# Kernel optimization log

Hardware: AMD Instinct MI355X
Metric: run time of the kernel (lower is better)

## Reference

```python
import jax, jax.numpy as jnp
import numpy as np

D = 1024        # embed_size
F = 4096        # ffn_dim
E = 8           # n_experts
K = 2           # top_k_experts
NS = 1          # n_shared
T = 8192        # tokens


def setup_inputs() -> dict:
    key = jax.random.key(0)
    ks = jax.random.split(key, 12)
    s = lambda *sh: 1.0 / np.sqrt(sh[-2] if len(sh) > 1 else sh[-1])
    inp = {
        "x": jax.random.normal(ks[0], (T, D), jnp.float32),
        "gate_w": jax.random.normal(ks[1], (D, E), jnp.float32) * (1.0 / np.sqrt(D)),
        "gate_b": jnp.zeros((E,), jnp.float32),
        "shared_w1": jax.random.normal(ks[2], (NS, D, 2 * F), jnp.float32) * (1.0 / np.sqrt(D)),
        "shared_b1": jnp.zeros((NS, 2 * F), jnp.float32),
        "shared_w2": jax.random.normal(ks[3], (NS, F, D), jnp.float32) * (1.0 / np.sqrt(F)),
        "shared_b2": jnp.zeros((NS, D), jnp.float32),
        "routed_w1": jax.random.normal(ks[4], (E, D, 2 * F), jnp.float32) * (1.0 / np.sqrt(D)),
        "routed_b1": jnp.zeros((E, 2 * F), jnp.float32),
        "routed_w2": jax.random.normal(ks[5], (E, F, D), jnp.float32) * (1.0 / np.sqrt(F)),
        "routed_b2": jnp.zeros((E, D), jnp.float32),
    }
    return inp


def _expert(x, w1, b1, w2, b2):
    # SwiGLU FFN: w2( silu(a) * b ) where [a, b] = chunk(x @ w1 + b1)
    h = x @ w1 + b1                      # [T, 2F]
    a, b = jnp.split(h, 2, axis=-1)      # [T, F] each
    return (jax.nn.silu(a) * b) @ w2 + b2  # [T, D]


def reference(x, gate_w, gate_b, shared_w1, shared_b1, shared_w2, shared_b2,
              routed_w1, routed_b1, routed_w2, routed_b2):
    # shared experts (always active)
    shared_out = jnp.zeros_like(x)
    for i in range(NS):
        shared_out = shared_out + _expert(x, shared_w1[i], shared_b1[i], shared_w2[i], shared_b2[i])

    # softmax gating + top-k selection
    logits = x @ gate_w + gate_b                      # [T, E]
    probs = jax.nn.softmax(logits, axis=-1)
    topk_probs, topk_idx = jax.lax.top_k(probs, K)    # [T, K]

    # per-token combine weight for each expert: sum_k p_k * 1[idx_k == e]
    one_hot = jax.nn.one_hot(topk_idx, E, dtype=x.dtype)        # [T, K, E]
    combine = jnp.einsum("tk,tke->te", topk_probs, one_hot)     # [T, E]

    # dispatch/combine: dense per-expert FFN, weighted by combine (zero off-route)
    routed_out = jnp.zeros_like(x)
    for e in range(E):
        y = _expert(x, routed_w1[e], routed_b1[e], routed_w2[e], routed_b2[e])
        routed_out = routed_out + y * combine[:, e:e + 1]

    return shared_out + routed_out
```

## Files before the change

kernel.cpp:

```cpp
#include <hip/hip_runtime.h>

#define TOK   8192
#define DD    1024
#define FF    4096
#define EE    8
#define TWOF  8192
#define NSLOT 16384
#define PADT  17408

typedef unsigned short u16;
typedef float  f32x16 __attribute__((ext_vector_type(16)));
typedef __bf16 bf16x8 __attribute__((ext_vector_type(8)));

__device__ __forceinline__ u16 f2b(float f) {
  unsigned u = __builtin_bit_cast(unsigned, f);
  u += 0x7fffu + ((u >> 16) & 1u);
  return (u16)(u >> 16);
}

__device__ __forceinline__ float b2f(u16 b) {
  return __builtin_bit_cast(float, (unsigned)b << 16);
}

__device__ __forceinline__ void ldslds16(const void* g, void* l) {
  __builtin_amdgcn_global_load_lds((const __attribute__((address_space(1))) void*)g,
                                   (__attribute__((address_space(3))) void*)l, 16, 0, 0);
}

__global__ void gate_kernel(const float* __restrict__ x, const float* __restrict__ gw,
                            const float* __restrict__ gb, int* __restrict__ counts,
                            int* __restrict__ eidx, int* __restrict__ epos,
                            float* __restrict__ ew, u16* __restrict__ xb) {
  const int wave = threadIdx.x >> 6, lane = threadIdx.x & 63;
  const int t = blockIdx.x * 4 + wave;
  float acc[EE] = {0,0,0,0,0,0,0,0};
  const float* xr = x + (size_t)t * DD;
  u16* xbr = xb + (size_t)t * DD;
#pragma unroll
  for (int i = 0; i < DD / 256; ++i) {
    const int f = i * 64 + lane;
    const float4 v = ((const float4*)xr)[f];
    const int d = f * 4;
    const float* g = gw + (size_t)d * EE;
#pragma unroll
    for (int e = 0; e < EE; ++e)
      acc[e] += v.x * g[e] + v.y * g[EE + e] + v.z * g[2 * EE + e] + v.w * g[3 * EE + e];
    uint2 pk;
    pk.x = (unsigned)f2b(v.x) | ((unsigned)f2b(v.y) << 16);
    pk.y = (unsigned)f2b(v.z) | ((unsigned)f2b(v.w) << 16);
    ((uint2*)xbr)[f] = pk;
  }
#pragma unroll
  for (int e = 0; e < EE; ++e)
#pragma unroll
    for (int off = 32; off > 0; off >>= 1) acc[e] += __shfl_down(acc[e], off);
  if (lane == 0) {
    float l[EE];
#pragma unroll
    for (int e = 0; e < EE; ++e) l[e] = acc[e] + gb[e];
    int i0 = 0;
    for (int e = 1; e < EE; ++e) if (l[e] > l[i0]) i0 = e;
    int i1 = (i0 == 0) ? 1 : 0;
    for (int e = 0; e < EE; ++e) { if (e == i0) continue; if (l[e] > l[i1]) i1 = e; }
    float m = l[0];
    for (int e = 1; e < EE; ++e) m = fmaxf(m, l[e]);
    float s = 0.f, p[EE];
    for (int e = 0; e < EE; ++e) { p[e] = __expf(l[e] - m); s += p[e]; }
    float w0 = p[i0] / s, w1 = p[i1] / s;
    int p0 = atomicAdd(&counts[i0], 1);
    int p1 = atomicAdd(&counts[i1], 1);
    eidx[2*t] = i0; eidx[2*t+1] = i1;
    epos[2*t] = p0; epos[2*t+1] = p1;
    ew[2*t] = w0;  ew[2*t+1] = w1;
  }
}

__global__ void slot_kernel(const int* __restrict__ eidx, const int* __restrict__ epos,
                            const float* __restrict__ ew, const int* __restrict__ counts,
                            int* __restrict__ s2t, float* __restrict__ swt,
                            int* __restrict__ t2s) {
  int i = blockIdx.x * 256 + threadIdx.x;
  int e = eidx[i];
  int off = 0;
  for (int j = 0; j < e; ++j) off += (counts[j] + 127) & ~127;
  int slot = off + epos[i];
  s2t[slot] = i >> 1;
  swt[slot] = ew[i];
  t2s[i] = slot;
}

__global__ void wt_kernel(const float* __restrict__ srcS, const float* __restrict__ srcR,
                          u16* __restrict__ dst, int K, int N, int permute) {
  __shared__ float tile[64][65];
  const int seg = blockIdx.z;
  const float* src = (seg == 0) ? srcS : srcR + (size_t)(seg - 1) * K * N;
  const int pc0 = blockIdx.x * 64, k0 = blockIdx.y * 64;
  const int tid = threadIdx.x;
  {
    const int kk = tid >> 2;
    const float* srow = src + (size_t)(k0 + kk) * N;
#pragma unroll
    for (int c4 = 0; c4 < 4; ++c4) {
      const int j = (tid & 3) * 4 + c4 * 16;
      const int n = pc0 + j;
      const int oc = permute ? (((n >> 6) << 5) + (n & 31) + ((n & 32) ? FF : 0)) : n;
      const float4 v = *(const float4*)(srow + oc);
      tile[kk][j]     = v.x; tile[kk][j + 1] = v.y;
      tile[kk][j + 2] = v.z; tile[kk][j + 3] = v.w;
    }
  }
  __syncthreads();
  {
    const int c = tid & 7;
#pragma unroll
    for (int p = 0; p < 2; ++p) {
      const int pp = p * 32 + (tid >> 3);
      u16* drow = dst + (size_t)seg * N * K + (size_t)(pc0 + pp) * K + k0;
      uint4 v; unsigned* pv = (unsigned*)&v;
#pragma unroll
      for (int q = 0; q < 4; ++q)
        pv[q] = (unsigned)f2b(tile[c * 8 + 2 * q][pp]) |
                ((unsigned)f2b(tile[c * 8 + 2 * q + 1][pp]) << 16);
      *(uint4*)(drow + c * 8) = v;
    }
  }
}


__device__ __forceinline__ void kloop32(int niter,
    const char* a0, const char* a1, const char* a2, const char* a3,
    const char* b0, const char* b1, const char* b2, const char* b3,
    u16* As, u16* Bs, int tid, f32x16 (&acc)[2][2]) {
  const int lane = tid & 63, l31 = lane & 31, kg = (lane >> 5) * 16;
  const int wid = tid >> 6, wm = wid >> 1, wn = wid & 1;
  const int C = (l31 & 7) << 4;
  const char* rA[4]; const char* rB[4];
#pragma unroll
  for (int ks = 0; ks < 4; ++ks) {
    const int o = (ks * 32 + kg) ^ C;
    rA[ks] = (const char*)As + (wm * 64 + l31) * 128 + o;
    rB[ks] = (const char*)Bs + (wn * 64 + l31) * 128 + o;
  }
  for (int it = 0; it < niter; ++it) {
    const long long kb = (long long)it * 128;
    ldslds16(a0 + kb, As + tid * 8);
    ldslds16(a1 + kb, As + 2048 + tid * 8);
    ldslds16(a2 + kb, As + 4096 + tid * 8);
    ldslds16(a3 + kb, As + 6144 + tid * 8);
    ldslds16(b0 + kb, Bs + tid * 8);
    ldslds16(b1 + kb, Bs + 2048 + tid * 8);
    ldslds16(b2 + kb, Bs + 4096 + tid * 8);
    ldslds16(b3 + kb, Bs + 6144 + tid * 8);
    __syncthreads();
#pragma unroll
    for (int ks = 0; ks < 4; ++ks) {
      bf16x8 af0 = *(const bf16x8*)(rA[ks]);
      bf16x8 af1 = *(const bf16x8*)(rA[ks] + 4096);
      bf16x8 bq0 = *(const bf16x8*)(rB[ks]);
      bf16x8 bq1 = *(const bf16x8*)(rB[ks] + 4096);
      acc[0][0] = __builtin_amdgcn_mfma_f32_32x32x16_bf16(af0, bq0, acc[0][0], 0, 0, 0);
      acc[0][1] = __builtin_amdgcn_mfma_f32_32x32x16_bf16(af0, bq1, acc[0][1], 0, 0, 0);
      acc[1][0] = __builtin_amdgcn_mfma_f32_32x32x16_bf16(af1, bq0, acc[1][0], 0, 0, 0);
      acc[1][1] = __builtin_amdgcn_mfma_f32_32x32x16_bf16(af1, bq1, acc[1][1], 0, 0, 0);
    }
    __syncthreads();
  }
}

__device__ __forceinline__ bool seg_map(int g, const int* __restrict__ counts,
                                        int& seg, int& tm, int& rowstart, int& rows) {
  if (g < 64) { seg = 0; tm = g; rowstart = 0; rows = TOK; return true; }
  int gr = g - 64, off = 0;
  for (int e = 0; e < EE; ++e) {
    int c = counts[e];
    int nb = (c + 127) >> 7;
    if (gr < nb) { seg = e + 1; tm = gr; rowstart = off; rows = c; return true; }
    gr -= nb;
    off += (c + 127) & ~127;
  }
  return false;
}

__global__ __launch_bounds__(256, 4)
void gemm1_kernel(const u16* __restrict__ xb, const int* __restrict__ s2t,
                  const u16* __restrict__ w1t, const float* __restrict__ sb1,
                  const float* __restrict__ rb1, const int* __restrict__ counts,
                  u16* __restrict__ hs) {
  __shared__ __align__(16) u16 As[128 * 64];
  __shared__ __align__(16) u16 Bs[128 * 64];
  const int lin = blockIdx.x + 64 * blockIdx.y;
  const int tn = (lin & 7) * 8 + ((lin >> 3) & 7);
  const int g = lin >> 6;
  int seg, tm, rowstart, rows;
  if (!seg_map(g, counts, seg, tm, rowstart, rows)) return;
  const int hsbase = (seg == 0) ? 0 : TOK + rowstart;
  const int tid = threadIdx.x, lane = tid & 63, wid = tid >> 6;
  const int wm = wid >> 1, wn = wid & 1;

  const int srow = tid >> 3;
  const int scol = ((tid & 7) * 16) ^ ((srow & 7) << 4);
  const char* Ac = (const char*)xb;
  const char* Bc = (const char*)(w1t + (size_t)seg * TWOF * DD);
  const char* a[4]; const char* b[4];
#pragma unroll
  for (int r = 0; r < 4; ++r) {
    int rbase = tm * 128 + r * 32 + srow;
    int rg = (seg == 0) ? rbase : s2t[rowstart + rbase];
    a[r] = Ac + (size_t)rg * (DD * 2) + scol;
    b[r] = Bc + (size_t)(tn * 128 + r * 32 + srow) * (DD * 2) + scol;
  }

  f32x16 acc[2][2] = {};
  kloop32(DD / 64, a[0], a[1], a[2], a[3], b[0], b[1], b[2], b[3],
          As, Bs, tid, acc);

  const int l31 = lane & 31, lg = lane >> 5;
  const int rlim = rows - tm * 128;
  const float* b1 = (seg == 0) ? sb1 : rb1 + (size_t)(seg - 1) * TWOF;
  const int f = (tn * 2 + wn) * 32 + l31;
  const float ba = b1[f], bb = b1[FF + f];
  u16* hbase = hs + (size_t)(hsbase + tm * 128) * FF;
#pragma unroll
  for (int mi = 0; mi < 2; ++mi)
#pragma unroll
    for (int reg = 0; reg < 16; ++reg) {
      int lr = wm * 64 + mi * 32 + (reg & 3) + 8 * (reg >> 2) + 4 * lg;
      if (lr < rlim) {
        float av = acc[mi][0][reg] + ba;
        float bv = acc[mi][1][reg] + bb;
        float sv = av / (1.0f + __expf(-av)) * bv;
        hbase[(size_t)lr * FF + f] = f2b(sv);
      }
    }
}

__global__ __launch_bounds__(256, 4)
void gemm2_kernel(const u16* __restrict__ hs, const u16* __restrict__ w2t,
                  const float* __restrict__ sb2, const float* __restrict__ rb2,
                  const int* __restrict__ counts, u16* __restrict__ yo) {
  __shared__ __align__(16) u16 As[128 * 64];
  __shared__ __align__(16) u16 Bs[128 * 64];
  const int tn = blockIdx.x;
  const int g = blockIdx.y;
  int seg, tm, rowstart, rows;
  if (!seg_map(g, counts, seg, tm, rowstart, rows)) return;
  const int hrow0 = (seg == 0) ? 0 : TOK + rowstart;
  const int tid = threadIdx.x, lane = tid & 63, wid = tid >> 6;
  const int wm = wid >> 1, wn = wid & 1;

  const int srow = tid >> 3;
  const int scol = ((tid & 7) * 16) ^ ((srow & 7) << 4);
  const char* Ac = (const char*)hs;
  const char* Bc = (const char*)(w2t + (size_t)seg * DD * FF);
  const char* a[4]; const char* b[4];
#pragma unroll
  for (int r = 0; r < 4; ++r) {
    a[r] = Ac + (size_t)(hrow0 + tm * 128 + r * 32 + srow) * (FF * 2) + scol;
    b[r] = Bc + (size_t)(tn * 128 + r * 32 + srow) * (FF * 2) + scol;
  }

  f32x16 acc[2][2] = {};
  kloop32(FF / 64, a[0], a[1], a[2], a[3], b[0], b[1], b[2], b[3],
          As, Bs, tid, acc);

  const int l31 = lane & 31, lg = lane >> 5;
  const int rlim = rows - tm * 128;
  const float* b2 = (seg == 0) ? sb2 : rb2 + (size_t)(seg - 1) * DD;
  const int c0 = tn * 128 + wn * 64 + l31;
  const float bias0 = b2[c0], bias1 = b2[c0 + 32];
  u16* ybase = yo + (size_t)(hrow0 + tm * 128) * DD;
#pragma unroll
  for (int mi = 0; mi < 2; ++mi)
#pragma unroll
    for (int reg = 0; reg < 16; ++reg) {
      int lr = wm * 64 + mi * 32 + (reg & 3) + 8 * (reg >> 2) + 4 * lg;
      if (lr < rlim) {
        u16* orow = ybase + (size_t)lr * DD;
        orow[c0]      = f2b(acc[mi][0][reg] + bias0);
        orow[c0 + 32] = f2b(acc[mi][1][reg] + bias1);
      }
    }
}

__global__ void combine_kernel(const u16* __restrict__ yo, const int* __restrict__ t2s,
                               const float* __restrict__ ew, float* __restrict__ out) {
  const int t = blockIdx.x, d = threadIdx.x;
  const int s0 = t2s[2*t], s1 = t2s[2*t+1];
  const float w0 = ew[2*t], w1 = ew[2*t+1];
  const uint2 pa = ((const uint2*)(yo + (size_t)t * DD))[d];
  const uint2 p0 = ((const uint2*)(yo + (size_t)(TOK + s0) * DD))[d];
  const uint2 p1 = ((const uint2*)(yo + (size_t)(TOK + s1) * DD))[d];
  float4 r;
  r.x = b2f((u16)pa.x)         + w0 * b2f((u16)p0.x)         + w1 * b2f((u16)p1.x);
  r.y = b2f((u16)(pa.x >> 16)) + w0 * b2f((u16)(p0.x >> 16)) + w1 * b2f((u16)(p1.x >> 16));
  r.z = b2f((u16)pa.y)         + w0 * b2f((u16)p0.y)         + w1 * b2f((u16)p1.y);
  r.w = b2f((u16)(pa.y >> 16)) + w0 * b2f((u16)(p0.y >> 16)) + w1 * b2f((u16)(p1.y >> 16));
  ((float4*)(out + (size_t)t * DD))[d] = r;
}

extern "C" void kernel_launch(void* const* d_in, const int* in_sizes, int n_in,
                              void* d_out, int out_size, void* d_ws, size_t ws_size,
                              hipStream_t stream) {
  const float* x   = (const float*)d_in[0];
  const float* gw  = (const float*)d_in[1];
  const float* gb  = (const float*)d_in[2];
  const float* sw1 = (const float*)d_in[3];
  const float* sb1 = (const float*)d_in[4];
  const float* sw2 = (const float*)d_in[5];
  const float* sb2 = (const float*)d_in[6];
  const float* rw1 = (const float*)d_in[7];
  const float* rb1 = (const float*)d_in[8];
  const float* rw2 = (const float*)d_in[9];
  const float* rb2 = (const float*)d_in[10];
  float* out = (float*)d_out;

  char* p = (char*)d_ws;
  auto alloc = [&](size_t bytes) { char* r = p; p += (bytes + 255) & ~(size_t)255; return r; };
  int*   counts = (int*)alloc(EE * 4);
  int*   eidx   = (int*)alloc((size_t)2 * TOK * 4);
  int*   epos   = (int*)alloc((size_t)2 * TOK * 4);
  float* ew     = (float*)alloc((size_t)2 * TOK * 4);
  int*   s2t    = (int*)alloc((size_t)PADT * 4);
  float* swt    = (float*)alloc((size_t)PADT * 4);
  int*   t2s    = (int*)alloc((size_t)2 * TOK * 4);
  u16*   xb     = (u16*)alloc((size_t)TOK * DD * 2);
  u16*   w1t    = (u16*)alloc((size_t)9 * TWOF * DD * 2);
  u16*   w2t    = (u16*)alloc((size_t)9 * DD * FF * 2);
  u16*   hs     = (u16*)alloc((size_t)(TOK + PADT + 128) * FF * 2);
  u16*   yo     = (u16*)w1t;

  hipMemsetAsync(counts, 0, EE * 4, stream);
  hipMemsetAsync(s2t, 0, (size_t)PADT * 4, stream);
  gate_kernel<<<TOK / 4, 256, 0, stream>>>(x, gw, gb, counts, eidx, epos, ew, xb);
  slot_kernel<<<(2 * TOK) / 256, 256, 0, stream>>>(eidx, epos, ew, counts, s2t, swt, t2s);
  wt_kernel<<<dim3(TWOF / 64, DD / 64, 9), 256, 0, stream>>>(sw1, rw1, w1t, DD, TWOF, 1);
  wt_kernel<<<dim3(DD / 64, FF / 64, 9), 256, 0, stream>>>(sw2, rw2, w2t, FF, DD, 0);
  gemm1_kernel<<<dim3(64, 200), 256, 0, stream>>>(xb, s2t, w1t, sb1, rb1, counts, hs);
  gemm2_kernel<<<dim3(8, 200), 256, 0, stream>>>(hs, w2t, sb2, rb2, counts, yo);
  combine_kernel<<<TOK, 256, 0, stream>>>(yo, t2s, ew, out);
}
```

Measured before the change: 1.079 ms.

## Switch GEMM inner loops from 32x32x16 to 16x16x32 bf16 MFMA tiles

Replaces the 32x32x16 MFMA micro-kernel with a 4x4 grid of 16x16x32 MFMA tiles per wave. The LDS fragment addressing, the SwiGLU column permutation in the weight pre-transpose, and both GEMM epilogues change to match the new accumulator layout. Each wave now issues more fragment loads and more, smaller MFMA instructions per K step, trading instruction count and register layout against MFMA issue characteristics. The permute has to stay consistent with the epilogue pairing of a and b columns.

```diff
diff --git a/kernel.cpp b/kernel.cpp
--- a/kernel.cpp
+++ b/kernel.cpp
@@ -9,7 +9,7 @@
 #define PADT  17408
 
 typedef unsigned short u16;
-typedef float  f32x16 __attribute__((ext_vector_type(16)));
+typedef float  f32x4  __attribute__((ext_vector_type(4)));
 typedef __bf16 bf16x8 __attribute__((ext_vector_type(8)));
 
 __device__ __forceinline__ u16 f2b(float f) {
@@ -103,7 +103,7 @@
     for (int c4 = 0; c4 < 4; ++c4) {
       const int j = (tid & 3) * 4 + c4 * 16;
       const int n = pc0 + j;
-      const int oc = permute ? (((n >> 6) << 5) + (n & 31) + ((n & 32) ? FF : 0)) : n;
+      const int oc = permute ? (((n >> 5) << 4) + (n & 15) + ((n & 16) ? FF : 0)) : n;
       const float4 v = *(const float4*)(srow + oc);
       tile[kk][j]     = v.x; tile[kk][j + 1] = v.y;
       tile[kk][j + 2] = v.z; tile[kk][j + 3] = v.w;
@@ -127,41 +127,46 @@
 }
 
 
-__device__ __forceinline__ void kloop32(int niter,
+__device__ __forceinline__ void kloop16(int niter,
     const char* a0, const char* a1, const char* a2, const char* a3,
     const char* b0, const char* b1, const char* b2, const char* b3,
-    u16* As, u16* Bs, int tid, f32x16 (&acc)[2][2]) {
-  const int lane = tid & 63, l31 = lane & 31, kg = (lane >> 5) * 16;
+    u16* As, u16* Bs, int tid, f32x4 (&acc)[4][4]) {
+  const int lane = tid & 63, fr = lane & 15, kb = (lane >> 4) * 16;
   const int wid = tid >> 6, wm = wid >> 1, wn = wid & 1;
-  const int C = (l31 & 7) << 4;
-  const char* rA[4]; const char* rB[4];
-#pragma unroll
-  for (int ks = 0; ks < 4; ++ks) {
-    const int o = (ks * 32 + kg) ^ C;
-    rA[ks] = (const char*)As + (wm * 64 + l31) * 128 + o;
-    rB[ks] = (const char*)Bs + (wn * 64 + l31) * 128 + o;
+  const int swz = (fr & 7) << 4;
+  const char* rA[2][4]; const char* rB[2][4];
+#pragma unroll
+  for (int ks = 0; ks < 2; ++ks) {
+    const int o = (ks * 64 + kb) ^ swz;
+#pragma unroll
+    for (int q = 0; q < 4; ++q) {
+      rA[ks][q] = (const char*)As + (wm * 64 + q * 16 + fr) * 128 + o;
+      rB[ks][q] = (const char*)Bs + (wn * 64 + q * 16 + fr) * 128 + o;
+    }
   }
   for (int it = 0; it < niter; ++it) {
-    const long long kb = (long long)it * 128;
-    ldslds16(a0 + kb, As + tid * 8);
-    ldslds16(a1 + kb, As + 2048 + tid * 8);
-    ldslds16(a2 + kb, As + 4096 + tid * 8);
-    ldslds16(a3 + kb, As + 6144 + tid * 8);
-    ldslds16(b0 + kb, Bs + tid * 8);
-    ldslds16(b1 + kb, Bs + 2048 + tid * 8);
-    ldslds16(b2 + kb, Bs + 4096 + tid * 8);
-    ldslds16(b3 + kb, Bs + 6144 + tid * 8);
+    const long long kbb = (long long)it * 128;
+    ldslds16(a0 + kbb, As + tid * 8);
+    ldslds16(a1 + kbb, As + 2048 + tid * 8);
+    ldslds16(a2 + kbb, As + 4096 + tid * 8);
+    ldslds16(a3 + kbb, As + 6144 + tid * 8);
+    ldslds16(b0 + kbb, Bs + tid * 8);
+    ldslds16(b1 + kbb, Bs + 2048 + tid * 8);
+    ldslds16(b2 + kbb, Bs + 4096 + tid * 8);
+    ldslds16(b3 + kbb, Bs + 6144 + tid * 8);
     __syncthreads();
 #pragma unroll
-    for (int ks = 0; ks < 4; ++ks) {
-      bf16x8 af0 = *(const bf16x8*)(rA[ks]);
-      bf16x8 af1 = *(const bf16x8*)(rA[ks] + 4096);
-      bf16x8 bq0 = *(const bf16x8*)(rB[ks]);
-      bf16x8 bq1 = *(const bf16x8*)(rB[ks] + 4096);
-      acc[0][0] = __builtin_amdgcn_mfma_f32_32x32x16_bf16(af0, bq0, acc[0][0], 0, 0, 0);
-      acc[0][1] = __builtin_amdgcn_mfma_f32_32x32x16_bf16(af0, bq1, acc[0][1], 0, 0, 0);
-      acc[1][0] = __builtin_amdgcn_mfma_f32_32x32x16_bf16(af1, bq0, acc[1][0], 0, 0, 0);
-      acc[1][1] = __builtin_amdgcn_mfma_f32_32x32x16_bf16(af1, bq1, acc[1][1], 0, 0, 0);
+    for (int ks = 0; ks < 2; ++ks) {
+      bf16x8 af[4], bq[4];
+#pragma unroll
+      for (int q = 0; q < 4; ++q) af[q] = *(const bf16x8*)(rA[ks][q]);
+#pragma unroll
+      for (int q = 0; q < 4; ++q) bq[q] = *(const bf16x8*)(rB[ks][q]);
+#pragma unroll
+      for (int mi = 0; mi < 4; ++mi)
+#pragma unroll
+        for (int ni = 0; ni < 4; ++ni)
+          acc[mi][ni] = __builtin_amdgcn_mfma_f32_16x16x32_bf16(af[mi], bq[ni], acc[mi][ni], 0, 0, 0);
     }
     __syncthreads();
   }
@@ -210,28 +215,33 @@
     b[r] = Bc + (size_t)(tn * 128 + r * 32 + srow) * (DD * 2) + scol;
   }
 
-  f32x16 acc[2][2] = {};
-  kloop32(DD / 64, a[0], a[1], a[2], a[3], b[0], b[1], b[2], b[3],
+  f32x4 acc[4][4] = {};
+  kloop16(DD / 64, a[0], a[1], a[2], a[3], b[0], b[1], b[2], b[3],
           As, Bs, tid, acc);
 
-  const int l31 = lane & 31, lg = lane >> 5;
+  const int fr = lane & 15;
   const int rlim = rows - tm * 128;
+  const int rb = wm * 64 + (lane >> 4) * 4;
   const float* b1 = (seg == 0) ? sb1 : rb1 + (size_t)(seg - 1) * TWOF;
-  const int f = (tn * 2 + wn) * 32 + l31;
-  const float ba = b1[f], bb = b1[FF + f];
   u16* hbase = hs + (size_t)(hsbase + tm * 128) * FF;
-#pragma unroll
-  for (int mi = 0; mi < 2; ++mi)
-#pragma unroll
-    for (int reg = 0; reg < 16; ++reg) {
-      int lr = wm * 64 + mi * 32 + (reg & 3) + 8 * (reg >> 2) + 4 * lg;
-      if (lr < rlim) {
-        float av = acc[mi][0][reg] + ba;
-        float bv = acc[mi][1][reg] + bb;
-        float sv = av / (1.0f + __expf(-av)) * bv;
-        hbase[(size_t)lr * FF + f] = f2b(sv);
+  const int fc = tn * 64 + wn * 32 + fr;
+#pragma unroll
+  for (int np = 0; np < 2; ++np) {
+    const int f = fc + np * 16;
+    const float ba = b1[f], bb = b1[FF + f];
+#pragma unroll
+    for (int m = 0; m < 4; ++m)
+#pragma unroll
+      for (int q = 0; q < 4; ++q) {
+        int lr = rb + m * 16 + q;
+        if (lr < rlim) {
+          float av = acc[m][2*np][q] + ba;
+          float bv = acc[m][2*np+1][q] + bb;
+          float sv = av / (1.0f + __expf(-av)) * bv;
+          hbase[(size_t)lr * FF + f] = f2b(sv);
+        }
       }
-    }
+  }
 }
 
 __global__ __launch_bounds__(256, 4)
@@ -259,26 +269,28 @@
     b[r] = Bc + (size_t)(tn * 128 + r * 32 + srow) * (FF * 2) + scol;
   }
 
-  f32x16 acc[2][2] = {};
-  kloop32(FF / 64, a[0], a[1], a[2], a[3], b[0], b[1], b[2], b[3],
+  f32x4 acc[4][4] = {};
+  kloop16(FF / 64, a[0], a[1], a[2], a[3], b[0], b[1], b[2], b[3],
           As, Bs, tid, acc);
 
-  const int l31 = lane & 31, lg = lane >> 5;
+  const int fr = lane & 15;
   const int rlim = rows - tm * 128;
+  const int rb = wm * 64 + (lane >> 4) * 4;
   const float* b2 = (seg == 0) ? sb2 : rb2 + (size_t)(seg - 1) * DD;
-  const int c0 = tn * 128 + wn * 64 + l31;
-  const float bias0 = b2[c0], bias1 = b2[c0 + 32];
+  const int cc = tn * 128 + wn * 64 + fr;
+  float bias[4];
+#pragma unroll
+  for (int n = 0; n < 4; ++n) bias[n] = b2[cc + n * 16];
   u16* ybase = yo + (size_t)(hrow0 + tm * 128) * DD;
 #pragma unroll
-  for (int mi = 0; mi < 2; ++mi)
-#pragma unroll
-    for (int reg = 0; reg < 16; ++reg) {
-      int lr = wm * 64 + mi * 32 + (reg & 3) + 8 * (reg >> 2) + 4 * lg;
-      if (lr < rlim) {
-        u16* orow = ybase + (size_t)lr * DD;
-        orow[c0]      = f2b(acc[mi][0][reg] + bias0);
-        orow[c0 + 32] = f2b(acc[mi][1][reg] + bias1);
-      }
+  for (int m = 0; m < 4; ++m)
+#pragma unroll
+    for (int q = 0; q < 4; ++q) {
+      int lr = rb + m * 16 + q;
+      if (lr >= rlim) continue;
+      u16* orow = ybase + (size_t)lr * DD;
+#pragma unroll
+      for (int n = 0; n < 4; ++n) orow[cc + n * 16] = f2b(acc[m][n][q] + bias[n]);
     }
 }
 
```

New measurement: 1.073 ms. Within noise of the previous version (-0.6%).
